# Kernel tuning notes

Hardware: AMD Instinct MI355X
Metric: run time of the kernel (lower is better)

The kernel has to match this reference:

```python
import jax, jax.numpy as jnp
import numpy as np

C_SOL = 299792458.0  # speed of light (m/s)


def setup_inputs() -> dict:
    key = jax.random.key(0)
    k1, k2 = jax.random.split(key, 2)
    K, T, R, N = 16, 8, 8, 32
    NX, NY, NZ = 64, 64, 32
    freqs = jnp.linspace(75e9, 80e9, K).astype(jnp.float32)
    # MIMO aperture: tx / rx linear arrays in the z=0 plane
    tx_positions = jnp.stack(
        [jnp.linspace(-0.15, 0.15, T), jnp.full((T,), -0.05), jnp.zeros((T,))], axis=-1
    ).astype(jnp.float32)
    rx_positions = jnp.stack(
        [jnp.linspace(-0.15, 0.15, R), jnp.full((R,), 0.05), jnp.zeros((R,))], axis=-1
    ).astype(jnp.float32)
    # imaging volume in front of the array (z >= 0.2 m, so ranges never vanish)
    x_coords = jnp.linspace(-0.2, 0.2, NX).astype(jnp.float32)
    y_coords = jnp.linspace(-0.2, 0.2, NY).astype(jnp.float32)
    z_coords = jnp.linspace(0.2, 0.5, NZ).astype(jnp.float32)
    y_real = jax.random.normal(k1, (N, 1, K, T, R), dtype=jnp.float32)
    y_imag = jax.random.normal(k2, (N, 1, K, T, R), dtype=jnp.float32)
    return {
        "freqs": freqs,
        "tx_positions": tx_positions,
        "rx_positions": rx_positions,
        "x_coords": x_coords,
        "y_coords": y_coords,
        "z_coords": z_coords,
        "y_real": y_real,
        "y_imag": y_imag,
    }


def _kirchhoff(freqs, tx_positions, rx_positions, x_coords, y_coords, z_coords, y_real, y_imag):
    ks = (2.0 * jnp.pi / C_SOL) * freqs  # (K,)
    # scene grid (NX, NY, NZ, 3)
    Xg, Yg, Zg = jnp.meshgrid(x_coords, y_coords, z_coords, indexing="ij")
    scene = jnp.stack([Xg, Yg, Zg], axis=-1)

    def ranges(pos):  # pos: (P, 3) -> (P, NX, NY, NZ)
        d = scene[None, ...] - pos[:, None, None, None, :]
        return jnp.sqrt(jnp.sum(d * d, axis=-1))

    R_tx = ranges(tx_positions)  # (T, NX, NY, NZ)
    R_rx = ranges(rx_positions)  # (R, NX, NY, NZ)
    z = scene[..., 2]
    dRtx_dz = (z[None] - tx_positions[:, 2][:, None, None, None]) / R_tx
    dRrx_dz = (z[None] - rx_positions[:, 2][:, None, None, None]) / R_rx

    Rsum = R_tx[:, None] + R_rx[None, :]   # (T, R, NX, NY, NZ)
    Rprod = R_tx[:, None] * R_rx[None, :]  # (T, R, NX, NY, NZ)
    g = 4.0 * dRtx_dz[:, None] * dRrx_dz[None, :]  # (T, R, NX, NY, NZ)

    y = (y_real + 1j * y_imag).astype(jnp.complex64)  # (N, 1, K, T, R)
    y_per_k = jnp.moveaxis(y, 2, 0)  # (K, N, 1, T, R)

    N, C = y.shape[0], y.shape[1]
    NX, NY, NZ = z.shape
    x0 = jnp.zeros((N, C, NX, NY, NZ), dtype=jnp.complex64)

    def step(x_acc, inp):
        k, y_k = inp  # k: scalar, y_k: (N, 1, T, R)
        phase = k * Rsum
        # R_rx*R_tx*(1j k)^2 + (R_rx+R_tx)*(1j k) + 1 = 1 - k^2*Rprod + 1j*k*Rsum
        A_k = g * (1.0 - (k * k) * Rprod + 1j * phase) * jnp.exp(1j * phase)
        x_acc = x_acc + jnp.einsum("trxyz,nctr->ncxyz", A_k.astype(jnp.complex64), y_k)
        return x_acc, None

    x, _ = jax.lax.scan(step, x0, (ks, y_per_k))
    return x  # (N, 1, NX, NY, NZ) complex64


def reference(freqs, tx_positions, rx_positions, x_coords, y_coords, z_coords, y_real, y_imag):
    x = _kirchhoff(freqs, tx_positions, rx_positions, x_coords, y_coords, z_coords, y_real, y_imag)
    mag = jnp.abs(x)
    return mag / jnp.max(mag)  # get_estimate(): abs(x / maxmag3D(x))
```

## Files before the change

### kernel.cpp

```cpp
#include <hip/hip_runtime.h>
#include <math.h>

namespace {
constexpr int K = 16, T = 8, R = 8, NB = 32;
constexpr int NX = 64, NY = 64, NZ = 32;
constexpr int NVOX = NX * NY * NZ;
constexpr float TWO_PI_OVER_C = (float)(6.283185307179586 / 299792458.0);
constexpr float CT_SCALE = 4.0f / 256.0f;
constexpr float CR_SCALE = 1.0f / 256.0f;
constexpr int B_HALVES = 64 * 3 * 2 * 32 * 8;
constexpr size_t WS_NEED = 256 + (size_t)B_HALVES * 2;
}

typedef _Float16 half8 __attribute__((ext_vector_type(8)));
typedef __fp16 fp16x2 __attribute__((ext_vector_type(2)));
typedef float f32x16 __attribute__((ext_vector_type(16)));

__global__ void prep_kernel(const float* __restrict__ yr, const float* __restrict__ yi,
                            _Float16* __restrict__ wsB, unsigned int* __restrict__ maxslot,
                            int use_ws) {
    int id = blockIdx.x * 256 + threadIdx.x;
    if (id == 0) *maxslot = 0u;
    if (!use_ws || id >= 64 * 3 * 2 * 32) return;
    int n    = id & 31;
    int rest = id >> 5;
    int kc   = rest & 1;
    int ftr  = rest >> 1;
    int f    = ftr % 3;
    int tr   = ftr / 3;
    int t = tr >> 3, r = tr & 7;
    const float* src = (f == 0) ? yr : yi;
    float sg = (f == 2) ? -1.0f : 1.0f;
    int base = n * (K * T * R) + (kc * 8) * (T * R) + t * R + r;
    half8 h;
#pragma unroll
    for (int j = 0; j < 8; ++j)
        h[j] = (_Float16)(sg * src[base + j * (T * R)]);
    ((half8*)wsB)[id] = h;
}

template <bool USE_WS>
__global__ __launch_bounds__(256, 3) void kirch_mfma(
    const float* __restrict__ freqs,
    const float* __restrict__ txp, const float* __restrict__ rxp,
    const float* __restrict__ xc, const float* __restrict__ yc, const float* __restrict__ zc,
    const _Float16* __restrict__ wsB,
    const float* __restrict__ yr, const float* __restrict__ yi,
    float* __restrict__ out, unsigned int* __restrict__ maxslot)
{
    __shared__ float s_wmax[4];

    const int tid  = threadIdx.x;
    const int lane = tid & 63;
    const int wave = tid >> 6;
    const int ml   = lane & 31;
    const int kc   = lane >> 5;
    const int vb   = blockIdx.x * 128 + wave * 32;
    const int v    = vb + ml;

    const float k0 = TWO_PI_OVER_C * freqs[0];
    const float dk = TWO_PI_OVER_C * (freqs[K - 1] - freqs[0]) * (1.0f / (K - 1));
    const float kstart = k0 + (float)(kc * 8) * dk;

    const float px = xc[v >> 11];
    const float py = yc[(v >> 5) & 63];
    const float pz = zc[v & 31];

    auto computeH = [&](float sx, float sy, float sz, float scale, half8& oRe, half8& oIm) {
        const float dx = px - sx, dy = py - sy, dz = pz - sz;
        const float Rr = sqrtf(dx * dx + dy * dy + dz * dz);
        const float c = scale * dz * __builtin_amdgcn_rcpf(Rr);
        float sph, cph, swp, cwp;
        __sincosf(kstart * Rr, &sph, &cph);
        __sincosf(dk * Rr, &swp, &cwp);
        float ur = cph, ui = sph;
        float ck = c * (kstart * Rr);
        const float dck = c * (dk * Rr);
        float hre[8], him[8];
#pragma unroll
        for (int j = 0; j < 8; ++j) {
            hre[j] = fmaf(c, ur, -(ck * ui));
            him[j] = fmaf(c, ui,  (ck * ur));
            if (j < 7) {
                float nr = fmaf(ur, cwp, -(ui * swp));
                ui = fmaf(ur, swp, ui * cwp);
                ur = nr;
                ck += dck;
            }
        }
        union { half8 v8; fp16x2 v2[4]; } uRe, uIm;
#pragma unroll
        for (int i = 0; i < 4; ++i) {
            uRe.v2[i] = __builtin_amdgcn_cvt_pkrtz(hre[2 * i], hre[2 * i + 1]);
            uIm.v2[i] = __builtin_amdgcn_cvt_pkrtz(him[2 * i], him[2 * i + 1]);
        }
        oRe = uRe.v8;
        oIm = uIm.v8;
    };

    half8 hrRe[8], hrIm[8];
#pragma unroll
    for (int r = 0; r < 8; ++r)
        computeH(rxp[r * 3 + 0], rxp[r * 3 + 1], rxp[r * 3 + 2], CR_SCALE, hrRe[r], hrIm[r]);

    f32x16 accRe = {0,0,0,0,0,0,0,0,0,0,0,0,0,0,0,0};
    f32x16 accIm = {0,0,0,0,0,0,0,0,0,0,0,0,0,0,0,0};

    const char* bbase = (const char*)wsB + kc * 512 + ml * 16;

    half8 bRe[2], bIm[2], bNi[2];
    auto loadB = [&](int buf, int tr) {
        if constexpr (USE_WS) {
            const char* bp = bbase + tr * 3072;
            bRe[buf] = *(const half8*)(bp);
            bIm[buf] = *(const half8*)(bp + 1024);
            bNi[buf] = *(const half8*)(bp + 2048);
        } else {
            int t = tr >> 3, r = tr & 7;
            int base = ml * (K * T * R) + (kc * 8) * (T * R) + t * R + r;
            half8 a, b, c2;
#pragma unroll
            for (int j = 0; j < 8; ++j) {
                float vre = yr[base + j * (T * R)];
                float vim = yi[base + j * (T * R)];
                a[j]  = (_Float16)vre;
                b[j]  = (_Float16)vim;
                c2[j] = (_Float16)(-vim);
            }
            bRe[buf] = a; bIm[buf] = b; bNi[buf] = c2;
        }
    };

    half8 htRe[2], htIm[2];
    computeH(txp[0], txp[1], txp[2], CT_SCALE, htRe[0], htIm[0]);
    loadB(0, 0);

#pragma unroll
    for (int it = 0; it < 64; ++it) {
        const int t   = it >> 3;
        const int r   = it & 7;
        const int cur = it & 1;
        const int nxt = cur ^ 1;

        if (it + 1 < 64) loadB(nxt, it + 1);
        if (r == 4 && t < 7)
            computeH(txp[(t + 1) * 3 + 0], txp[(t + 1) * 3 + 1], txp[(t + 1) * 3 + 2],
                     CT_SCALE, htRe[(t + 1) & 1], htIm[(t + 1) & 1]);

        half8 hRe = htRe[t & 1], hIm = htIm[t & 1];
        half8 ARe = hRe * hrRe[r] - hIm * hrIm[r];
        half8 AIm = hRe * hrIm[r] + hIm * hrRe[r];

        accRe = __builtin_amdgcn_mfma_f32_32x32x16_f16(ARe, bRe[cur], accRe, 0, 0, 0);
        accIm = __builtin_amdgcn_mfma_f32_32x32x16_f16(ARe, bIm[cur], accIm, 0, 0, 0);
        accRe = __builtin_amdgcn_mfma_f32_32x32x16_f16(AIm, bNi[cur], accRe, 0, 0, 0);
        accIm = __builtin_amdgcn_mfma_f32_32x32x16_f16(AIm, bRe[cur], accIm, 0, 0, 0);
    }

    float mx = 0.0f;
#pragma unroll
    for (int g = 0; g < 4; ++g) {
        float om[4];
#pragma unroll
        for (int e = 0; e < 4; ++e) {
            float re = accRe[4 * g + e], im = accIm[4 * g + e];
            float m = sqrtf(re * re + im * im);
            om[e] = m;
            mx = fmaxf(mx, m);
        }
        *(float4*)&out[ml * NVOX + vb + 8 * g + 4 * kc] = *(float4*)om;
    }
#pragma unroll
    for (int off = 32; off > 0; off >>= 1)
        mx = fmaxf(mx, __shfl_down(mx, off));
    if (lane == 0) s_wmax[wave] = mx;
    __syncthreads();
    if (tid == 0) {
        float bm = fmaxf(fmaxf(s_wmax[0], s_wmax[1]), fmaxf(s_wmax[2], s_wmax[3]));
        atomicMax(maxslot, __float_as_uint(bm));
    }
}

__global__ void normalize_kernel(float* __restrict__ out,
                                 const unsigned int* __restrict__ maxslot, int n4) {
    int i = blockIdx.x * blockDim.x + threadIdx.x;
    float inv = 1.0f / __uint_as_float(*maxslot);
    if (i < n4) {
        float4* o = (float4*)out;
        float4 vv = o[i];
        vv.x *= inv; vv.y *= inv; vv.z *= inv; vv.w *= inv;
        o[i] = vv;
    }
}

extern "C" void kernel_launch(void* const* d_in, const int* in_sizes, int n_in,
                              void* d_out, int out_size, void* d_ws, size_t ws_size,
                              hipStream_t stream) {
    const float* freqs = (const float*)d_in[0];
    const float* txp   = (const float*)d_in[1];
    const float* rxp   = (const float*)d_in[2];
    const float* xc    = (const float*)d_in[3];
    const float* yc    = (const float*)d_in[4];
    const float* zc    = (const float*)d_in[5];
    const float* yr    = (const float*)d_in[6];
    const float* yi    = (const float*)d_in[7];
    float* out = (float*)d_out;

    unsigned int* maxslot = (unsigned int*)d_ws;
    _Float16* wsB = (_Float16*)((char*)d_ws + 256);
    const int use_ws = (ws_size >= WS_NEED) ? 1 : 0;

    prep_kernel<<<48, 256, 0, stream>>>(yr, yi, wsB, maxslot, use_ws);

    if (use_ws)
        kirch_mfma<true><<<NVOX / 128, 256, 0, stream>>>(
            freqs, txp, rxp, xc, yc, zc, wsB, yr, yi, out, maxslot);
    else
        kirch_mfma<false><<<NVOX / 128, 256, 0, stream>>>(
            freqs, txp, rxp, xc, yc, zc, wsB, yr, yi, out, maxslot);

    int n4 = out_size / 4;
    normalize_kernel<<<(n4 + 255) / 256, 256, 0, stream>>>(out, maxslot, n4);
}
```

Measured before the change: 130.0 us.

## Split tx/rx reduction across wave pairs and combine partial sums in LDS

Each block now covers 64 voxels with two waves per 32-voxel tile; each wave of a pair handles half the transmitters (32 of 64 tx-rx pairs), and the partial MFMA accumulators are summed through shared memory before the magnitude and max step. This doubles the grid and halves the serial MFMA chain per wave, giving more parallelism and occupancy (launch bounds raised to 4 blocks). In exchange, the receiver phasor setup is done twice per voxel tile, and the kernel gains LDS traffic, extra barriers and one atomicMax per pair rather than per block.

```diff
diff --git a/kernel.cpp b/kernel.cpp
--- a/kernel.cpp
+++ b/kernel.cpp
@@ -40,7 +40,7 @@
 }
 
 template <bool USE_WS>
-__global__ __launch_bounds__(256, 3) void kirch_mfma(
+__global__ __launch_bounds__(256, 4) void kirch_mfma(
     const float* __restrict__ freqs,
     const float* __restrict__ txp, const float* __restrict__ rxp,
     const float* __restrict__ xc, const float* __restrict__ yc, const float* __restrict__ zc,
@@ -48,14 +48,16 @@
     const float* __restrict__ yr, const float* __restrict__ yi,
     float* __restrict__ out, unsigned int* __restrict__ maxslot)
 {
-    __shared__ float s_wmax[4];
+    __shared__ float sAcc[2][16][64];
 
     const int tid  = threadIdx.x;
     const int lane = tid & 63;
     const int wave = tid >> 6;
+    const int pair = wave >> 1;
+    const int half = wave & 1;
     const int ml   = lane & 31;
     const int kc   = lane >> 5;
-    const int vb   = blockIdx.x * 128 + wave * 32;
+    const int vb   = blockIdx.x * 64 + pair * 32;
     const int v    = vb + ml;
 
     const float k0 = TWO_PI_OVER_C * freqs[0];
@@ -106,16 +108,18 @@
     f32x16 accRe = {0,0,0,0,0,0,0,0,0,0,0,0,0,0,0,0};
     f32x16 accIm = {0,0,0,0,0,0,0,0,0,0,0,0,0,0,0,0};
 
-    const char* bbase = (const char*)wsB + kc * 512 + ml * 16;
+    const int tr0 = half * 32;
+    const char* bbase = (const char*)wsB + (size_t)tr0 * 3072 + kc * 512 + ml * 16;
 
     half8 bRe[2], bIm[2], bNi[2];
-    auto loadB = [&](int buf, int tr) {
+    auto loadB = [&](int buf, int it) {
         if constexpr (USE_WS) {
-            const char* bp = bbase + tr * 3072;
+            const char* bp = bbase + it * 3072;
             bRe[buf] = *(const half8*)(bp);
             bIm[buf] = *(const half8*)(bp + 1024);
             bNi[buf] = *(const half8*)(bp + 2048);
         } else {
+            int tr = tr0 + it;
             int t = tr >> 3, r = tr & 7;
             int base = ml * (K * T * R) + (kc * 8) * (T * R) + t * R + r;
             half8 a, b, c2;
@@ -132,22 +136,27 @@
     };
 
     half8 htRe[2], htIm[2];
-    computeH(txp[0], txp[1], txp[2], CT_SCALE, htRe[0], htIm[0]);
+    {
+        const int t0 = half * 4;
+        computeH(txp[t0 * 3 + 0], txp[t0 * 3 + 1], txp[t0 * 3 + 2], CT_SCALE, htRe[0], htIm[0]);
+    }
     loadB(0, 0);
 
 #pragma unroll
-    for (int it = 0; it < 64; ++it) {
-        const int t   = it >> 3;
+    for (int it = 0; it < 32; ++it) {
+        const int tl  = it >> 3;
         const int r   = it & 7;
         const int cur = it & 1;
         const int nxt = cur ^ 1;
 
-        if (it + 1 < 64) loadB(nxt, it + 1);
-        if (r == 4 && t < 7)
-            computeH(txp[(t + 1) * 3 + 0], txp[(t + 1) * 3 + 1], txp[(t + 1) * 3 + 2],
-                     CT_SCALE, htRe[(t + 1) & 1], htIm[(t + 1) & 1]);
-
-        half8 hRe = htRe[t & 1], hIm = htIm[t & 1];
+        if (it + 1 < 32) loadB(nxt, it + 1);
+        if (r == 4 && tl < 3) {
+            const int tn = half * 4 + tl + 1;
+            computeH(txp[tn * 3 + 0], txp[tn * 3 + 1], txp[tn * 3 + 2],
+                     CT_SCALE, htRe[(tl + 1) & 1], htIm[(tl + 1) & 1]);
+        }
+
+        half8 hRe = htRe[tl & 1], hIm = htIm[tl & 1];
         half8 ARe = hRe * hrRe[r] - hIm * hrIm[r];
         half8 AIm = hRe * hrIm[r] + hIm * hrRe[r];
 
@@ -157,27 +166,43 @@
         accIm = __builtin_amdgcn_mfma_f32_32x32x16_f16(AIm, bRe[cur], accIm, 0, 0, 0);
     }
 
-    float mx = 0.0f;
-#pragma unroll
-    for (int g = 0; g < 4; ++g) {
-        float om[4];
-#pragma unroll
-        for (int e = 0; e < 4; ++e) {
-            float re = accRe[4 * g + e], im = accIm[4 * g + e];
-            float m = sqrtf(re * re + im * im);
-            om[e] = m;
-            mx = fmaxf(mx, m);
-        }
-        *(float4*)&out[ml * NVOX + vb + 8 * g + 4 * kc] = *(float4*)om;
-    }
-#pragma unroll
-    for (int off = 32; off > 0; off >>= 1)
-        mx = fmaxf(mx, __shfl_down(mx, off));
-    if (lane == 0) s_wmax[wave] = mx;
+    if (half == 1) {
+#pragma unroll
+        for (int e = 0; e < 16; ++e) sAcc[pair][e][lane] = accRe[e];
+    }
     __syncthreads();
-    if (tid == 0) {
-        float bm = fmaxf(fmaxf(s_wmax[0], s_wmax[1]), fmaxf(s_wmax[2], s_wmax[3]));
-        atomicMax(maxslot, __float_as_uint(bm));
+    if (half == 0) {
+#pragma unroll
+        for (int e = 0; e < 16; ++e) accRe[e] += sAcc[pair][e][lane];
+    }
+    __syncthreads();
+    if (half == 1) {
+#pragma unroll
+        for (int e = 0; e < 16; ++e) sAcc[pair][e][lane] = accIm[e];
+    }
+    __syncthreads();
+    if (half == 0) {
+#pragma unroll
+        for (int e = 0; e < 16; ++e) accIm[e] += sAcc[pair][e][lane];
+
+        float mx = 0.0f;
+#pragma unroll
+        for (int g = 0; g < 4; ++g) {
+            float om[4];
+#pragma unroll
+            for (int e = 0; e < 4; ++e) {
+                float re = accRe[4 * g + e], im = accIm[4 * g + e];
+                float m = sqrtf(re * re + im * im);
+                om[e] = m;
+                mx = fmaxf(mx, m);
+            }
+            *(float4*)&out[ml * NVOX + vb + 8 * g + 4 * kc] = *(float4*)om;
+        }
+#pragma unroll
+        for (int off = 32; off > 0; off >>= 1)
+            mx = fmaxf(mx, __shfl_down(mx, off));
+        if (lane == 0)
+            atomicMax(maxslot, __float_as_uint(mx));
     }
 }
 
@@ -213,10 +238,10 @@
     prep_kernel<<<48, 256, 0, stream>>>(yr, yi, wsB, maxslot, use_ws);
 
     if (use_ws)
-        kirch_mfma<true><<<NVOX / 128, 256, 0, stream>>>(
+        kirch_mfma<true><<<NVOX / 64, 256, 0, stream>>>(
             freqs, txp, rxp, xc, yc, zc, wsB, yr, yi, out, maxslot);
     else
-        kirch_mfma<false><<<NVOX / 128, 256, 0, stream>>>(
+        kirch_mfma<false><<<NVOX / 64, 256, 0, stream>>>(
             freqs, txp, rxp, xc, yc, zc, wsB, yr, yi, out, maxslot);
 
     int n4 = out_size / 4;
```

Measured after the change: 170.4 us. 1.31x slower.
